# Optimization experiments

Hardware: AMD Instinct MI355X
Metric: run time of the kernel (lower is better)

Reference implementation:

```python
import jax, jax.numpy as jnp
import numpy as np

TEMP = 0.5
LAMDA = 1.0
NUM_SLICE = 64
EPS = 1e-20


def _gaussian_kernel(size=11, sigma=1.5):
    coords = np.arange(size, dtype=np.float64) - (size - 1) / 2.0
    g = np.exp(-(coords ** 2) / (2.0 * sigma ** 2))
    g = g / g.sum()
    return jnp.asarray(g, dtype=jnp.float32)


def _ssim(x, y, data_range=1.0, win_size=11, sigma=1.5):
    # x, y: [B, S, H, W]; treat each slice as an independent 1-channel image.
    B, S, H, W = x.shape
    x4 = x.reshape(B * S, 1, H, W)
    y4 = y.reshape(B * S, 1, H, W)
    g = _gaussian_kernel(win_size, sigma)
    kh = g.reshape(1, 1, win_size, 1)
    kw = g.reshape(1, 1, 1, win_size)
    dn = ('NCHW', 'OIHW', 'NCHW')

    def blur(a):
        a = jax.lax.conv_general_dilated(a, kh, (1, 1), 'VALID', dimension_numbers=dn)
        a = jax.lax.conv_general_dilated(a, kw, (1, 1), 'VALID', dimension_numbers=dn)
        return a

    mu1 = blur(x4)
    mu2 = blur(y4)
    mu1_sq = mu1 * mu1
    mu2_sq = mu2 * mu2
    mu1_mu2 = mu1 * mu2
    sigma1_sq = blur(x4 * x4) - mu1_sq
    sigma2_sq = blur(y4 * y4) - mu2_sq
    sigma12 = blur(x4 * y4) - mu1_mu2
    C1 = (0.01 * data_range) ** 2
    C2 = (0.03 * data_range) ** 2
    ssim_map = ((2.0 * mu1_mu2 + C1) * (2.0 * sigma12 + C2)) / (
        (mu1_sq + mu2_sq + C1) * (sigma1_sq + sigma2_sq + C2))
    return jnp.mean(ssim_map)


def _l1(a, b):
    return jnp.mean(jnp.abs(a - b))


def _cumulative_mips(img_fake, target, gumbel, temp):
    # Growing-window gumbel-softmax MIP, computed in a single O(S) pass.
    # softmax over a prefix window is shift-invariant, so subtract the
    # per-pixel global max over the slice axis for stability, then use cumsums.
    y = img_fake + gumbel
    m = jnp.max(y, axis=1, keepdims=True)
    e = jnp.exp((y - m) / temp)                      # unnormalized softmax weights
    num = jnp.cumsum(e * img_fake, axis=1)
    den = jnp.cumsum(e, axis=1)
    pred_c1 = num / den                              # prefix windows [0:idx+1]
    target_c1 = jax.lax.cummax(target, axis=1)

    ef = jnp.flip(e, axis=1)
    xf = jnp.flip(img_fake, axis=1)
    num2 = jnp.cumsum(ef * xf, axis=1)
    den2 = jnp.cumsum(ef, axis=1)
    pred_c2 = num2 / den2                            # suffix windows [S-1-idx:]
    target_c2 = jax.lax.cummax(jnp.flip(target, axis=1), axis=1)
    return pred_c1, target_c1, pred_c2, target_c2


def _forward(img_fake, target, u_noise):
    gumbel = -jnp.log(-jnp.log(u_noise + EPS) + EPS)
    p1, t1, p2, t2 = _cumulative_mips(img_fake, target, gumbel, TEMP)
    loss_lissim = (_l1(img_fake, target) + 1.0 - _ssim(img_fake, target)) * LAMDA
    loss_mip_c1 = (_l1(p1, t1) + 1.0 - _ssim(p1, t1)) * LAMDA
    loss_mip_c2 = (_l1(p2, t2) + 1.0 - _ssim(p2, t2)) * LAMDA
    return loss_lissim + loss_mip_c1 + loss_mip_c2


def setup_inputs() -> dict:
    key = jax.random.key(0)
    k1, k2, k3 = jax.random.split(key, 3)
    shape = (2, NUM_SLICE, 256, 256)
    img_fake = jax.random.uniform(k1, shape, dtype=jnp.float32)
    target = jax.random.uniform(k2, shape, dtype=jnp.float32)
    u_noise = jax.random.uniform(k3, shape, dtype=jnp.float32)
    return {"img_fake": img_fake, "target": target, "u_noise": u_noise}


def reference(img_fake, target, u_noise):
    return _forward(img_fake, target, u_noise)
```

## Files before the change

### kernel.cpp

```cpp
#include <hip/hip_runtime.h>
#include <cmath>
#include <cstring>

#define NUM_S   64
#define IMG_H   256
#define IMG_W   256
#define HWSZ    (IMG_H*IMG_W)
#define BATCH   2
#define NPIX    (BATCH*HWSZ)
#define NEL     (BATCH*NUM_S*HWSZ)
#define NSLICE  (BATCH*NUM_S)
#define VALID   246
#define EPS_F   1e-20f
#define C1_F    1e-4f
#define C2_F    9e-4f
#define RS      264
#define FS      (16*RS)
#define NSLOT_SCAN 1024
#define NSLOT_ALL  7168
#define PTPAD   1024

typedef __fp16 half8  __attribute__((ext_vector_type(8)));
typedef __fp16 fp16x2 __attribute__((ext_vector_type(2)));
using fragC = __attribute__((ext_vector_type(4))) float;

union H8 { half8 v; short s[8]; int i[4]; };
union PK { fp16x2 v; int i; };
union HS { __fp16 f; short s; };

struct GH { short h[11]; };

__device__ inline fp16x2 pkrtz(float a, float b) {
    return __builtin_amdgcn_cvt_pkrtz(a, b);
}
__device__ inline float frcp(float x)  { return __builtin_amdgcn_rcpf(x); }
__device__ inline float flog2(float x) { return __builtin_amdgcn_logf(x); }
__device__ inline float fexp2(float x) { return __builtin_amdgcn_exp2f(x); }

__device__ inline void block_reduce_slot(float v, float* slot) {
    __shared__ float sm[8];
    __syncthreads();
    #pragma unroll
    for (int off = 32; off; off >>= 1) v += __shfl_down(v, off, 64);
    int lane = threadIdx.x & 63, w = threadIdx.x >> 6;
    if (lane == 0) sm[w] = v;
    __syncthreads();
    if (threadIdx.x == 0) {
        float s = 0.f;
        int nw = blockDim.x >> 6;
        for (int i = 0; i < nw; ++i) s += sm[i];
        *slot = s;
    }
}

__global__ __launch_bounds__(256) void scan_kernel(
    const float* __restrict__ img, const float* __restrict__ tgt,
    const float* __restrict__ un,
    uint2* __restrict__ pt0, uint2* __restrict__ pt1, uint2* __restrict__ pt2,
    float* __restrict__ slots, GH gh, unsigned short* __restrict__ bandTbl)
{
    if (blockIdx.x == 0 && threadIdx.x < 64) {
        int q = threadIdx.x >> 4, n = threadIdx.x & 15;
        #pragma unroll
        for (int j = 0; j < 8; ++j) {
            int kk = q * 8 + j - n;
            short hv = 0;
            #pragma unroll
            for (int w = 0; w < 11; ++w) hv = (kk == w) ? gh.h[w] : hv;
            bandTbl[threadIdx.x * 8 + j] = (unsigned short)hv;
        }
    }

    const int HW2 = HWSZ / 2;
    int tid = blockIdx.x * 256 + threadIdx.x;
    bool bwd = tid >= (NPIX / 2);
    int p2 = bwd ? tid - NPIX / 2 : tid;
    int b   = p2 >> 15;
    int hw2 = p2 & (HW2 - 1);
    int idx  = b * (NUM_S * HW2) + hw2 + (bwd ? (NUM_S - 1) * HW2 : 0);
    int step = bwd ? -HW2 : HW2;
    const float2* __restrict__ img2 = (const float2*)img;
    const float2* __restrict__ tgt2 = (const float2*)tgt;
    const float2* __restrict__ un2  = (const float2*)un;

    float num[2] = {0.f, 0.f}, den[2] = {0.f, 0.f}, tm[2] = {-INFINITY, -INFINITY};
    float l1x = 0.f, l1p = 0.f;

    float2 xb[4], ub[4], tb[4];
    #pragma unroll
    for (int j = 0; j < 4; ++j) {
        int id = idx + j * step;
        xb[j] = img2[id]; ub[j] = un2[id]; tb[j] = tgt2[id];
    }

    for (int i = 0; i < NUM_S; i += 4) {
        #pragma unroll
        for (int j = 0; j < 4; ++j) {
            float2 x = xb[j], u = ub[j], t = tb[j];
            if (i + j + 4 < NUM_S) {
                int id = idx + 4 * step;
                xb[j] = img2[id]; ub[j] = un2[id]; tb[j] = tgt2[id];
            }
            float xc[2] = {x.x, x.y}, uc[2] = {u.x, u.y}, tc[2] = {t.x, t.y};
            float p[2];
            #pragma unroll
            for (int c = 0; c < 2; ++c) {
                float w = fmaf(flog2(uc[c] + EPS_F), -0.6931471805599453f, EPS_F);
                float r = frcp(w);
                float e = fexp2(xc[c] * 2.8853900817779268f) * (r * r);
                num[c] = fmaf(e, xc[c], num[c]);
                den[c] += e;
                p[c] = num[c] * frcp(den[c]);
                tm[c] = fmaxf(tm[c], tc[c]);
                if (!bwd) l1x += fabsf(xc[c] - tc[c]);
                l1p += fabsf(p[c] - tm[c]);
            }
            PK k0, k1;
            k0.v = pkrtz(p[0], tm[0]); k1.v = pkrtz(p[1], tm[1]);
            uint2 pv = make_uint2((unsigned)k0.i, (unsigned)k1.i);
            if (!bwd) {
                PK a0, a1;
                a0.v = pkrtz(xc[0], tc[0]); a1.v = pkrtz(xc[1], tc[1]);
                pt0[idx] = make_uint2((unsigned)a0.i, (unsigned)a1.i);
                pt1[idx] = pv;
            } else {
                pt2[idx] = pv;
            }
            idx += step;
        }
    }
    block_reduce_slot(bwd ? 0.f : l1x, &slots[blockIdx.x]);
    block_reduce_slot(l1p, &slots[512 + blockIdx.x]);
}

__global__ __launch_bounds__(256) void ssim_kernel(
    const unsigned* __restrict__ pt0, const unsigned* __restrict__ pt1,
    const unsigned* __restrict__ pt2,
    const int4* __restrict__ bandTbl, float* __restrict__ slots)
{
    __shared__ short Vl[5][FS];
    int pair  = blockIdx.z;
    int yy    = blockIdx.y;
    int bsel  = yy & 1, ss = yy >> 1;
    int sy    = bsel * NUM_S + ((pair == 2) ? ss : (NUM_S - 1 - ss));
    int base  = sy * HWSZ;
    int r0    = blockIdx.x * 16;
    int lane  = threadIdx.x & 63;
    int wid   = threadIdx.x >> 6;
    int q     = lane >> 4;
    int n     = lane & 15;

    const unsigned* __restrict__ pp =
        (pair == 0 ? pt0 : (pair == 1 ? pt1 : pt2)) + base;
    bool clampR = (r0 == 240);
    const fragC zero = {0.f, 0.f, 0.f, 0.f};

    unsigned ld[32];
    {
        int rowbase = r0 + q * 8;
        if (!clampR) {
            const unsigned* pb = pp + rowbase * IMG_W + n;
            #pragma unroll
            for (int it = 0; it < 4; ++it)
                #pragma unroll
                for (int j = 0; j < 8; ++j)
                    ld[it * 8 + j] = pb[j * IMG_W + (wid * 4 + it) * 16];
        } else {
            #pragma unroll
            for (int it = 0; it < 4; ++it)
                #pragma unroll
                for (int j = 0; j < 8; ++j) {
                    int rr = min(rowbase + j, IMG_H - 1);
                    ld[it * 8 + j] = pp[rr * IMG_W + (wid * 4 + it) * 16 + n];
                }
        }
    }
    H8 band;
    *(int4*)band.i = bandTbl[lane];

    for (int d = threadIdx.x; d < 320; d += 256) {
        int f = d >> 6, rm = d & 63, r = rm >> 2, cc = rm & 3;
        ((int*)Vl)[f * 2112 + r * 132 + 128 + cc] = 0;
    }

    #pragma unroll
    for (int it = 0; it < 4; ++it) {
        H8 fX, fY, fXX, fYY, fXY;
        #pragma unroll
        for (int j = 0; j < 4; ++j) {
            unsigned a = ld[it * 8 + 2 * j], b2 = ld[it * 8 + 2 * j + 1];
            fX.i[j] = (int)((a & 0xffffu) | (b2 << 16));
            fY.i[j] = (int)((a >> 16) | (b2 & 0xffff0000u));
        }
        fXX.v = fX.v * fX.v;
        fYY.v = fY.v * fY.v;
        fXY.v = fX.v * fY.v;
        fragC v0 = __builtin_amdgcn_mfma_f32_16x16x32_f16(band.v, fX.v,  zero, 0, 0, 0);
        fragC v1 = __builtin_amdgcn_mfma_f32_16x16x32_f16(band.v, fY.v,  zero, 0, 0, 0);
        fragC v2 = __builtin_amdgcn_mfma_f32_16x16x32_f16(band.v, fXX.v, zero, 0, 0, 0);
        fragC v3 = __builtin_amdgcn_mfma_f32_16x16x32_f16(band.v, fYY.v, zero, 0, 0, 0);
        fragC v4 = __builtin_amdgcn_mfma_f32_16x16x32_f16(band.v, fXY.v, zero, 0, 0, 0);
        int col = (wid * 4 + it) * 16 + n;
        #pragma unroll
        for (int reg = 0; reg < 4; ++reg) {
            int ro = (q * 4 + reg) * RS + col;
            HS cv;
            cv.f = (__fp16)v0[reg]; Vl[0][ro] = cv.s;
            cv.f = (__fp16)v1[reg]; Vl[1][ro] = cv.s;
            cv.f = (__fp16)v2[reg]; Vl[2][ro] = cv.s;
            cv.f = (__fp16)v3[reg]; Vl[3][ro] = cv.s;
            cv.f = (__fp16)v4[reg]; Vl[4][ro] = cv.s;
        }
    }
    __syncthreads();

    float lsum = 0.f;
    for (int it = 0; it < 4; ++it) {
        int c0 = (wid * 4 + it) * 16;
        int so = n * RS + c0 + q * 8;
        so = min(so, FS - 8);
        H8 a0, a1, a2, a3, a4;
        *(int4*)a0.i = *(const int4*)&Vl[0][so];
        *(int4*)a1.i = *(const int4*)&Vl[1][so];
        *(int4*)a2.i = *(const int4*)&Vl[2][so];
        *(int4*)a3.i = *(const int4*)&Vl[3][so];
        *(int4*)a4.i = *(const int4*)&Vl[4][so];
        fragC o0 = __builtin_amdgcn_mfma_f32_16x16x32_f16(a0.v, band.v, zero, 0, 0, 0);
        fragC o1 = __builtin_amdgcn_mfma_f32_16x16x32_f16(a1.v, band.v, zero, 0, 0, 0);
        fragC o2 = __builtin_amdgcn_mfma_f32_16x16x32_f16(a2.v, band.v, zero, 0, 0, 0);
        fragC o3 = __builtin_amdgcn_mfma_f32_16x16x32_f16(a3.v, band.v, zero, 0, 0, 0);
        fragC o4 = __builtin_amdgcn_mfma_f32_16x16x32_f16(a4.v, band.v, zero, 0, 0, 0);
        #pragma unroll
        for (int reg = 0; reg < 4; ++reg) {
            int r = r0 + q * 4 + reg;
            int c = c0 + n;
            if (r < VALID && c < VALID) {
                float m1 = o0[reg], m2 = o1[reg];
                float s11 = o2[reg] - m1 * m1;
                float s22 = o3[reg] - m2 * m2;
                float s12 = o4[reg] - m1 * m2;
                float nv = (2.f * m1 * m2 + C1_F) * (2.f * s12 + C2_F);
                float dv = (m1 * m1 + m2 * m2 + C1_F) * (s11 + s22 + C2_F);
                lsum += nv * frcp(dv);
            }
        }
    }
    block_reduce_slot(lsum,
        &slots[NSLOT_SCAN + pair * 2048 + blockIdx.y * 16 + blockIdx.x]);
}

__global__ void finalize_kernel(const float* __restrict__ slots,
                                float* __restrict__ out) {
    __shared__ double sa[4], sb[4];
    double a = 0.0, bsum = 0.0;
    for (int i = threadIdx.x; i < NSLOT_SCAN; i += 256) a += (double)slots[i];
    for (int i = NSLOT_SCAN + threadIdx.x; i < NSLOT_ALL; i += 256) bsum += (double)slots[i];
    #pragma unroll
    for (int off = 32; off; off >>= 1) {
        a    += __shfl_down(a, off, 64);
        bsum += __shfl_down(bsum, off, 64);
    }
    int lane = threadIdx.x & 63, w = threadIdx.x >> 6;
    if (lane == 0) { sa[w] = a; sb[w] = bsum; }
    __syncthreads();
    if (threadIdx.x == 0) {
        double A = sa[0] + sa[1] + sa[2] + sa[3];
        double B = sb[0] + sb[1] + sb[2] + sb[3];
        out[0] = (float)(3.0 + A / (double)NEL -
                         B / ((double)NSLICE * (double)VALID * (double)VALID));
    }
}

static unsigned short f32_to_f16(float f) {
    unsigned u; memcpy(&u, &f, 4);
    unsigned s = (u >> 16) & 0x8000u;
    int e = (int)((u >> 23) & 0xff) - 127 + 15;
    unsigned m = u & 0x7fffffu;
    unsigned h = s | ((unsigned)e << 10) | (m >> 13);
    unsigned rem = m & 0x1fffu;
    if (rem > 0x1000u || (rem == 0x1000u && (h & 1))) h++;
    return (unsigned short)h;
}
static double f16_to_d(unsigned short h) {
    unsigned e = (h >> 10) & 0x1f, m = h & 0x3ffu;
    return ldexp((double)(m + 1024), (int)e - 25);
}

extern "C" void kernel_launch(void* const* d_in, const int* in_sizes, int n_in,
                              void* d_out, int out_size, void* d_ws, size_t ws_size,
                              hipStream_t stream) {
    const float* img = (const float*)d_in[0];
    const float* tgt = (const float*)d_in[1];
    const float* un  = (const float*)d_in[2];
    float* out = (float*)d_out;

    unsigned* pt0 = (unsigned*)d_ws;
    unsigned* pt1 = pt0 + NEL + PTPAD;
    unsigned* pt2 = pt1 + NEL + PTPAD;
    float* slots = (float*)(pt2 + NEL);
    unsigned short* bandTbl = (unsigned short*)(slots + NSLOT_ALL);

    GH gh;
    {
        double g[11], s = 0.0;
        for (int i = 0; i < 11; ++i) { double d = i - 5; g[i] = exp(-d * d / 4.5); s += g[i]; }
        for (int i = 0; i < 11; ++i) g[i] /= s;
        for (int iter = 0; iter < 3; ++iter) {
            double sb = 0.0;
            unsigned short h[11];
            for (int i = 0; i < 11; ++i) { h[i] = f32_to_f16((float)g[i]); sb += f16_to_d(h[i]); }
            for (int i = 0; i < 11; ++i) { g[i] /= sb; gh.h[i] = (short)h[i]; }
        }
    }

    scan_kernel<<<NPIX / 256, 256, 0, stream>>>(img, tgt, un,
        (uint2*)pt0, (uint2*)pt1, (uint2*)pt2, slots, gh, bandTbl);
    ssim_kernel<<<dim3(16, NSLICE, 3), 256, 0, stream>>>(pt0, pt1, pt2,
        (const int4*)bandTbl, slots);
    finalize_kernel<<<1, 256, 0, stream>>>(slots, out);
}
```

Measured before the change: 195.1 us.

## Offload pt0 packing and L1 to extra scan blocks; transpose MFMA for packed LDS stores

The scan kernel gains 128 extra blocks that pack image/target into pt0 and compute the plain L1 sum with a simple grid-stride loop. This removes that work and its divergent branch from the serial forward-scan threads, so forward and backward scan threads now do the same amount of work. The vertical-blur MFMA operands are swapped so each lane holds four contiguous outputs, which are stored to LDS as one packed 8-byte write instead of scalar 2-byte stores. The slot layout is re-indexed to match. The extra blocks reread img and tgt from memory.

```diff
diff --git a/kernel.cpp b/kernel.cpp
--- a/kernel.cpp
+++ b/kernel.cpp
@@ -16,8 +16,9 @@
 #define C2_F    9e-4f
 #define RS      264
 #define FS      (16*RS)
-#define NSLOT_SCAN 1024
-#define NSLOT_ALL  7168
+#define NSCANB  640
+#define SS_BASE 1280
+#define NSLOT_ALL  7424
 #define PTPAD   1024
 
 typedef __fp16 half8  __attribute__((ext_vector_type(8)));
@@ -26,7 +27,6 @@
 
 union H8 { half8 v; short s[8]; int i[4]; };
 union PK { fp16x2 v; int i; };
-union HS { __fp16 f; short s; };
 
 struct GH { short h[11]; };
 
@@ -59,7 +59,8 @@
     uint2* __restrict__ pt0, uint2* __restrict__ pt1, uint2* __restrict__ pt2,
     float* __restrict__ slots, GH gh, unsigned short* __restrict__ bandTbl)
 {
-    if (blockIdx.x == 0 && threadIdx.x < 64) {
+    int bid = blockIdx.x;
+    if (bid == 0 && threadIdx.x < 64) {
         int q = threadIdx.x >> 4, n = threadIdx.x & 15;
         #pragma unroll
         for (int j = 0; j < 8; ++j) {
@@ -71,8 +72,25 @@
         }
     }
 
+    if (bid >= 512) {
+        const float2* __restrict__ img2 = (const float2*)img;
+        const float2* __restrict__ tgt2 = (const float2*)tgt;
+        int t0 = (bid - 512) * 256 + threadIdx.x;
+        float l1x = 0.f;
+        for (int i = t0; i < NEL / 2; i += 128 * 256) {
+            float2 a = img2[i], b = tgt2[i];
+            PK a0, a1;
+            a0.v = pkrtz(a.x, b.x); a1.v = pkrtz(a.y, b.y);
+            pt0[i] = make_uint2((unsigned)a0.i, (unsigned)a1.i);
+            l1x += fabsf(a.x - b.x) + fabsf(a.y - b.y);
+        }
+        block_reduce_slot(l1x, &slots[bid]);
+        block_reduce_slot(0.f, &slots[NSCANB + bid]);
+        return;
+    }
+
     const int HW2 = HWSZ / 2;
-    int tid = blockIdx.x * 256 + threadIdx.x;
+    int tid = bid * 256 + threadIdx.x;
     bool bwd = tid >= (NPIX / 2);
     int p2 = bwd ? tid - NPIX / 2 : tid;
     int b   = p2 >> 15;
@@ -82,9 +100,10 @@
     const float2* __restrict__ img2 = (const float2*)img;
     const float2* __restrict__ tgt2 = (const float2*)tgt;
     const float2* __restrict__ un2  = (const float2*)un;
+    uint2* __restrict__ pt = bwd ? pt2 : pt1;
 
     float num[2] = {0.f, 0.f}, den[2] = {0.f, 0.f}, tm[2] = {-INFINITY, -INFINITY};
-    float l1x = 0.f, l1p = 0.f;
+    float l1p = 0.f;
 
     float2 xb[4], ub[4], tb[4];
     #pragma unroll
@@ -112,25 +131,16 @@
                 den[c] += e;
                 p[c] = num[c] * frcp(den[c]);
                 tm[c] = fmaxf(tm[c], tc[c]);
-                if (!bwd) l1x += fabsf(xc[c] - tc[c]);
                 l1p += fabsf(p[c] - tm[c]);
             }
             PK k0, k1;
             k0.v = pkrtz(p[0], tm[0]); k1.v = pkrtz(p[1], tm[1]);
-            uint2 pv = make_uint2((unsigned)k0.i, (unsigned)k1.i);
-            if (!bwd) {
-                PK a0, a1;
-                a0.v = pkrtz(xc[0], tc[0]); a1.v = pkrtz(xc[1], tc[1]);
-                pt0[idx] = make_uint2((unsigned)a0.i, (unsigned)a1.i);
-                pt1[idx] = pv;
-            } else {
-                pt2[idx] = pv;
-            }
+            pt[idx] = make_uint2((unsigned)k0.i, (unsigned)k1.i);
             idx += step;
         }
     }
-    block_reduce_slot(bwd ? 0.f : l1x, &slots[blockIdx.x]);
-    block_reduce_slot(l1p, &slots[512 + blockIdx.x]);
+    block_reduce_slot(0.f, &slots[bid]);
+    block_reduce_slot(l1p, &slots[NSCANB + bid]);
 }
 
 __global__ __launch_bounds__(256) void ssim_kernel(
@@ -195,22 +205,23 @@
         fXX.v = fX.v * fX.v;
         fYY.v = fY.v * fY.v;
         fXY.v = fX.v * fY.v;
-        fragC v0 = __builtin_amdgcn_mfma_f32_16x16x32_f16(band.v, fX.v,  zero, 0, 0, 0);
-        fragC v1 = __builtin_amdgcn_mfma_f32_16x16x32_f16(band.v, fY.v,  zero, 0, 0, 0);
-        fragC v2 = __builtin_amdgcn_mfma_f32_16x16x32_f16(band.v, fXX.v, zero, 0, 0, 0);
-        fragC v3 = __builtin_amdgcn_mfma_f32_16x16x32_f16(band.v, fYY.v, zero, 0, 0, 0);
-        fragC v4 = __builtin_amdgcn_mfma_f32_16x16x32_f16(band.v, fXY.v, zero, 0, 0, 0);
-        int col = (wid * 4 + it) * 16 + n;
-        #pragma unroll
-        for (int reg = 0; reg < 4; ++reg) {
-            int ro = (q * 4 + reg) * RS + col;
-            HS cv;
-            cv.f = (__fp16)v0[reg]; Vl[0][ro] = cv.s;
-            cv.f = (__fp16)v1[reg]; Vl[1][ro] = cv.s;
-            cv.f = (__fp16)v2[reg]; Vl[2][ro] = cv.s;
-            cv.f = (__fp16)v3[reg]; Vl[3][ro] = cv.s;
-            cv.f = (__fp16)v4[reg]; Vl[4][ro] = cv.s;
-        }
+        fragC v0 = __builtin_amdgcn_mfma_f32_16x16x32_f16(fX.v,  band.v, zero, 0, 0, 0);
+        fragC v1 = __builtin_amdgcn_mfma_f32_16x16x32_f16(fY.v,  band.v, zero, 0, 0, 0);
+        fragC v2 = __builtin_amdgcn_mfma_f32_16x16x32_f16(fXX.v, band.v, zero, 0, 0, 0);
+        fragC v3 = __builtin_amdgcn_mfma_f32_16x16x32_f16(fYY.v, band.v, zero, 0, 0, 0);
+        fragC v4 = __builtin_amdgcn_mfma_f32_16x16x32_f16(fXY.v, band.v, zero, 0, 0, 0);
+        int ro = n * RS + (wid * 4 + it) * 16 + q * 4;
+        PK pa, pb;
+        pa.v = pkrtz(v0[0], v0[1]); pb.v = pkrtz(v0[2], v0[3]);
+        *(int2*)&Vl[0][ro] = make_int2(pa.i, pb.i);
+        pa.v = pkrtz(v1[0], v1[1]); pb.v = pkrtz(v1[2], v1[3]);
+        *(int2*)&Vl[1][ro] = make_int2(pa.i, pb.i);
+        pa.v = pkrtz(v2[0], v2[1]); pb.v = pkrtz(v2[2], v2[3]);
+        *(int2*)&Vl[2][ro] = make_int2(pa.i, pb.i);
+        pa.v = pkrtz(v3[0], v3[1]); pb.v = pkrtz(v3[2], v3[3]);
+        *(int2*)&Vl[3][ro] = make_int2(pa.i, pb.i);
+        pa.v = pkrtz(v4[0], v4[1]); pb.v = pkrtz(v4[2], v4[3]);
+        *(int2*)&Vl[4][ro] = make_int2(pa.i, pb.i);
     }
     __syncthreads();
 
@@ -246,15 +257,15 @@
         }
     }
     block_reduce_slot(lsum,
-        &slots[NSLOT_SCAN + pair * 2048 + blockIdx.y * 16 + blockIdx.x]);
+        &slots[SS_BASE + pair * 2048 + blockIdx.y * 16 + blockIdx.x]);
 }
 
 __global__ void finalize_kernel(const float* __restrict__ slots,
                                 float* __restrict__ out) {
     __shared__ double sa[4], sb[4];
     double a = 0.0, bsum = 0.0;
-    for (int i = threadIdx.x; i < NSLOT_SCAN; i += 256) a += (double)slots[i];
-    for (int i = NSLOT_SCAN + threadIdx.x; i < NSLOT_ALL; i += 256) bsum += (double)slots[i];
+    for (int i = threadIdx.x; i < SS_BASE; i += 256) a += (double)slots[i];
+    for (int i = SS_BASE + threadIdx.x; i < NSLOT_ALL; i += 256) bsum += (double)slots[i];
     #pragma unroll
     for (int off = 32; off; off >>= 1) {
         a    += __shfl_down(a, off, 64);
@@ -313,7 +324,7 @@
         }
     }
 
-    scan_kernel<<<NPIX / 256, 256, 0, stream>>>(img, tgt, un,
+    scan_kernel<<<NSCANB, 256, 0, stream>>>(img, tgt, un,
         (uint2*)pt0, (uint2*)pt1, (uint2*)pt2, slots, gh, bandTbl);
     ssim_kernel<<<dim3(16, NSLICE, 3), 256, 0, stream>>>(pt0, pt1, pt2,
         (const int4*)bandTbl, slots);
```

Measured after the change: 208.5 us. 1.07x slower.
